# Performance work log

Measured on AMD Instinct MI355X. Metric: run time of the kernel, lower is better.

## Reference

```python
import jax, jax.numpy as jnp
import numpy as np

# q_config constants
W_IN, E_IN = 8, 4          # data_in_width, data_in_exponent_width
R_W = 6                     # data_r_width
W_OUT, E_OUT = 8, 4        # data_out_width, data_out_exponent_width (= data_n_width)
EXP_SUM_UF = 4              # exp_sum_underflow_bits
DIV_UF = 4                  # division_underflow_bits
W_DATA, E_DATA = 8, 4      # data_width, data_exponent_width

N, D = 8192, 2048


def integer_quantizer(x, width, frac_width):
    s = 2.0 ** frac_width
    lo, hi = -(2.0 ** (width - 1)), 2.0 ** (width - 1) - 1
    return jnp.clip(jnp.round(x * s), lo, hi) / s


def integer_floor_quantizer(x, width, frac_width):
    s = 2.0 ** frac_width
    lo, hi = -(2.0 ** (width - 1)), 2.0 ** (width - 1) - 1
    return jnp.clip(jnp.floor(x * s), lo, hi) / s


def mxint_quant(x, width, exponent_width):
    # MXInt block quantization with parallelism [1,1]: per-element shared exponent.
    e_hi, e_lo = 2.0 ** (exponent_width - 1) - 1, -(2.0 ** (exponent_width - 1))
    ax = jnp.abs(x)
    e = jnp.ceil(jnp.log2(jnp.where(ax == 0, 1.0, ax)))
    e = jnp.clip(e, e_lo, e_hi)
    scale = 2.0 ** (width - 1)
    m = jnp.clip(jnp.round(x * 2.0 ** (-e) * scale), -scale, scale - 1)
    qx = m * 2.0 ** e / scale
    return qx, m, e


def setup_inputs() -> dict:
    key = jax.random.key(0)
    x = jax.random.normal(key, (N, D), dtype=jnp.float32)
    return {"x": x}


def reference(x):
    # ---- MXIntHardwareExp: quantize input, range-reduce x = r + n*ln2 ----
    qx, _, _ = mxint_quant(x, W_IN, E_IN)
    log2e, _, _ = mxint_quant(jnp.float32(np.log2(np.e)), 8, 4)
    y = qx * log2e
    y = integer_floor_quantizer(y, E_OUT + R_W - 1, R_W - 1)
    n = jnp.floor(y)
    r = y - n                                # r in [0, 1)
    mexp = integer_quantizer(2.0 ** r, W_OUT, W_OUT - 2) * 2.0 ** (W_OUT - 2)
    eexp = n                                 # qexp = mexp * 2^eexp / 2^(W_OUT-2)

    # ---- exp_sum: exponent-aligned integer accumulation over dim 1 ----
    ms = (mexp * 2.0 ** EXP_SUM_UF).T        # [D, N]
    es = eexp.T                              # [D, N]

    def step(carry, me):
        out, emax = carry
        mi, ei = me
        new_emax = jnp.maximum(emax, ei)
        out = jnp.floor(out * 2.0 ** (emax - new_emax)) + jnp.floor(mi * 2.0 ** (ei - new_emax))
        return (out, new_emax), None

    (mexp_sum, eexp_sum), _ = jax.lax.scan(step, (ms[0], es[0]), (ms[1:], es[1:]))
    # mexp_sum, eexp_sum: [N]

    # ---- division: per-element mantissa integer division by the sum ----
    mout = jnp.floor(mexp * 2.0 ** (DIV_UF + EXP_SUM_UF) / mexp_sum[:, None])
    eout = eexp - eexp_sum[:, None]
    qout = mout * 2.0 ** eout / 2.0 ** DIV_UF
    qout, _, _ = mxint_quant(qout, W_DATA, E_DATA)
    return qout
```

## Files before the change

### kernel.cpp

```cpp
#include <hip/hip_runtime.h>


#define D_DIM 2048
#define TPB   128

__device__ __forceinline__ unsigned bmax4(unsigned x, unsigned y) {
    const unsigned d     = (x | 0x80808080u) - y;
    const unsigned flags = d & 0x80808080u;
    const unsigned mask  = (flags - (flags >> 7)) | flags;
    return (x & mask) | (y & ~mask);
}

__global__ __launch_bounds__(TPB, 6) void mxint_softmax_kernel(const float* __restrict__ x,
                                                               float* __restrict__ out) {
    const int t    = threadIdx.x;
    const int lane = t & 63;
    const int wid  = t >> 6;

    __shared__ unsigned short     s_pk[512];
    __shared__ float              s_fin[2][512];
    __shared__ int                s_rmax[2];
    __shared__ unsigned long long s_part[2];

    const size_t base = (size_t)blockIdx.x * D_DIM + wid * 1024 + lane * 4;
    float4 v[4];
#pragma unroll
    for (int i = 0; i < 4; ++i)
        v[i] = *(const float4*)(x + base + i * 256);

#pragma unroll
    for (int q = 0; q < 4; ++q) {
        const int idx = t + TPB * q;
        const float a = fmaf((float)(idx & 31), 0.03125f, 6.0f);
        const int  me = (int)rintf(__builtin_amdgcn_exp2f(a));
        s_pk[idx] = (unsigned short)(me << 4);
    }

    int yb[16];
    unsigned pe = 0;
#pragma unroll
    for (int i = 0; i < 4; ++i) {
        const float xs4[4] = {v[i].x, v[i].y, v[i].z, v[i].w};
        int rmax = 0;
#pragma unroll
        for (int k = 0; k < 4; ++k) {
            const unsigned b  = __float_as_uint(xs4[k]) & 0x7fffffffu;
            const unsigned tb = b + 0x7fffffu;
            const unsigned tc = min(max(tb, 0x3B800000u), 0x43000000u);
            const unsigned es = tc & 0xFF800000u;
            const float    su  = __uint_as_float(0x82800000u - es);
            const float    fac = __uint_as_float(es + 0xFF380000u);
            const float    mi  = __builtin_amdgcn_fmed3f(rintf(xs4[k] * su), -128.0f, 127.0f);
            int y = (int)fmaf(mi, fac, 256.0f);
            y = min(511, max(0, y));
            yb[4 * i + k] = y;
            rmax = max(rmax, y);
        }
        pe |= (unsigned)(rmax >> 5) << (8 * i);
    }

    unsigned s = pe;
#pragma unroll
    for (int d = 1; d < 64; d <<= 1) {
        const unsigned o = __shfl_up(s, d, 64);
        if (lane >= d) s = bmax4(s, o);
    }
    unsigned ex = __shfl_up(s, 1, 64);
    if (lane == 0) ex = 0;
    const unsigned bc = __shfl(s, 63, 64);
    const int wtot = max(max((int)(bc & 255u), (int)((bc >> 8) & 255u)),
                         max((int)((bc >> 16) & 255u), (int)(bc >> 24)));
    if (lane == 0) s_rmax[wid] = wtot;
    __syncthreads();

    const int c0 = wid ? s_rmax[0] : 0;

    unsigned partial = 0;
    int crun = c0;
#pragma unroll
    for (int i = 0; i < 4; ++i) {
        const int sx = (int)((ex >> (8 * i)) & 255u);
        int a = max(crun, sx);
#pragma unroll
        for (int k = 0; k < 4; ++k) {
            const int y = yb[4 * i + k];
            const int h = y >> 5;
            a = max(a, h);
            const unsigned me4 = s_pk[y];
            partial += (me4 >> (a - h)) << a;
        }
        crun = max(crun, (int)((bc >> (8 * i)) & 255u));
    }

    const unsigned ps = partial + __shfl_xor(partial, 1, 64);
    unsigned long long p64 = ps;
#pragma unroll
    for (int d = 2; d < 64; d <<= 1) p64 += __shfl_xor(p64, d, 64);
    if (lane == 0) s_part[wid] = p64;
    __syncthreads();

    const unsigned long long tot = s_part[0] + s_part[1];
    const int      Estar8 = max(s_rmax[0], s_rmax[1]);
    const unsigned msum   = (unsigned)(tot >> Estar8);
    const unsigned magic  = (unsigned)(274877906944.0 / (double)msum) + 1u;

    float* fin = s_fin[wid];
#pragma unroll
    for (int q = 0; q < 8; ++q) {
        const int      idx   = lane + 64 * q;
        const unsigned me4   = s_pk[idx];
        const unsigned mout  = __umulhi((unsigned)me4 << 4, magic) >> 6;
        const int      eoutn = Estar8 - (idx >> 5);
        const int      bl    = 32 - __clz((int)(mout | 1u));
        const int      pw2   = ((mout & (mout - 1u)) == 0u) ? 1 : 0;
        const int      clog  = bl - pw2;
        const int      sq    = min(7 - clog, 11 - eoutn);
        const int      rs    = 8 - sq;
        const unsigned u     = mout << 8;
        const unsigned bse   = u >> rs;
        const unsigned frac  = u & ((1u << rs) - 1u);
        const unsigned hlf   = 1u << (rs - 1);
        unsigned m2 = bse + (((frac > hlf) || (frac == hlf && (bse & 1u))) ? 1u : 0u);
        m2 = min(m2, 127u);
        const int ef = max(clog - eoutn - 4, -8);
        fin[idx] = (float)m2 * __uint_as_float((unsigned)(ef + 120) << 23);
    }

    float* orow = out + base;
#pragma unroll
    for (int i = 0; i < 4; ++i) {
        float r4[4];
#pragma unroll
        for (int k = 0; k < 4; ++k)
            r4[k] = fin[yb[4 * i + k]];
        const float4 o4 = {r4[0], r4[1], r4[2], r4[3]};
        *(float4*)(orow + i * 256) = o4;
    }
}

extern "C" void kernel_launch(void* const* d_in, const int* in_sizes, int n_in,
                              void* d_out, int out_size, void* d_ws, size_t ws_size,
                              hipStream_t stream) {
    const float* x = (const float*)d_in[0];
    float*       o = (float*)d_out;
    const int rows = in_sizes[0] / D_DIM;
    mxint_softmax_kernel<<<rows, TPB, 0, stream>>>(x, o);
}
```

Measured before the change: 110.8 us.

## Process four rows per block with register prefetch of next row

The grid shrinks to a fixed 2048 blocks, each looping over four rows strided by the block count. While the current row is computed, the next row's float4 loads are issued into registers, and the lookup table is built once per block instead of once per row. The goal is to hide global load latency and cut per-block setup cost. In exchange, register pressure rises, launch bounds drop from 6 to 4 blocks per CU, and the row count is hardcoded rather than taken from the input size.

```diff
diff --git a/kernel.cpp b/kernel.cpp
--- a/kernel.cpp
+++ b/kernel.cpp
@@ -3,6 +3,8 @@
 
 #define D_DIM 2048
 #define TPB   128
+#define NBLK  2048
+#define RPB   4
 
 __device__ __forceinline__ unsigned bmax4(unsigned x, unsigned y) {
     const unsigned d     = (x | 0x80808080u) - y;
@@ -11,7 +13,7 @@
     return (x & mask) | (y & ~mask);
 }
 
-__global__ __launch_bounds__(TPB, 6) void mxint_softmax_kernel(const float* __restrict__ x,
+__global__ __launch_bounds__(TPB, 4) void mxint_softmax_kernel(const float* __restrict__ x,
                                                                float* __restrict__ out) {
     const int t    = threadIdx.x;
     const int lane = t & 63;
@@ -19,14 +21,18 @@
 
     __shared__ unsigned short     s_pk[512];
     __shared__ float              s_fin[2][512];
-    __shared__ int                s_rmax[2];
-    __shared__ unsigned long long s_part[2];
+    __shared__ int                s_rmax[2][2];
+    __shared__ unsigned long long s_part[2][2];
 
-    const size_t base = (size_t)blockIdx.x * D_DIM + wid * 1024 + lane * 4;
+    const size_t off = (size_t)wid * 1024 + (size_t)lane * 4;
+
     float4 v[4];
+    {
+        const float* xr = x + (size_t)blockIdx.x * D_DIM + off;
 #pragma unroll
-    for (int i = 0; i < 4; ++i)
-        v[i] = *(const float4*)(x + base + i * 256);
+        for (int i = 0; i < 4; ++i)
+            v[i] = *(const float4*)(xr + i * 256);
+    }
 
 #pragma unroll
     for (int q = 0; q < 4; ++q) {
@@ -36,105 +42,124 @@
         s_pk[idx] = (unsigned short)(me << 4);
     }
 
-    int yb[16];
-    unsigned pe = 0;
+    for (int r = 0; r < RPB; ++r) {
+        const int row = blockIdx.x + r * NBLK;
+        const int pr  = r & 1;
+
+        float4 vn[4];
+        if (r + 1 < RPB) {
+            const float* xn = x + (size_t)(row + NBLK) * D_DIM + off;
 #pragma unroll
-    for (int i = 0; i < 4; ++i) {
-        const float xs4[4] = {v[i].x, v[i].y, v[i].z, v[i].w};
-        int rmax = 0;
+            for (int i = 0; i < 4; ++i)
+                vn[i] = *(const float4*)(xn + i * 256);
+        }
+
+        int yb[16];
+        unsigned pe = 0;
 #pragma unroll
-        for (int k = 0; k < 4; ++k) {
-            const unsigned b  = __float_as_uint(xs4[k]) & 0x7fffffffu;
-            const unsigned tb = b + 0x7fffffu;
-            const unsigned tc = min(max(tb, 0x3B800000u), 0x43000000u);
-            const unsigned es = tc & 0xFF800000u;
-            const float    su  = __uint_as_float(0x82800000u - es);
-            const float    fac = __uint_as_float(es + 0xFF380000u);
-            const float    mi  = __builtin_amdgcn_fmed3f(rintf(xs4[k] * su), -128.0f, 127.0f);
-            int y = (int)fmaf(mi, fac, 256.0f);
-            y = min(511, max(0, y));
-            yb[4 * i + k] = y;
-            rmax = max(rmax, y);
+        for (int i = 0; i < 4; ++i) {
+            const float xs4[4] = {v[i].x, v[i].y, v[i].z, v[i].w};
+            int rmax = 0;
+#pragma unroll
+            for (int k = 0; k < 4; ++k) {
+                const unsigned b  = __float_as_uint(xs4[k]) & 0x7fffffffu;
+                const unsigned tb = b + 0x7fffffu;
+                const unsigned tc = min(max(tb, 0x3B800000u), 0x43000000u);
+                const unsigned es = tc & 0xFF800000u;
+                const float    su  = __uint_as_float(0x82800000u - es);
+                const float    fac = __uint_as_float(es + 0xFF380000u);
+                const float    mi  = __builtin_amdgcn_fmed3f(rintf(xs4[k] * su),
+                                                             -128.0f, 127.0f);
+                int y = (int)fmaf(mi, fac, 256.0f);
+                y = min(511, max(0, y));
+                yb[4 * i + k] = y;
+                rmax = max(rmax, y);
+            }
+            pe |= (unsigned)(rmax >> 5) << (8 * i);
         }
-        pe |= (unsigned)(rmax >> 5) << (8 * i);
-    }
 
-    unsigned s = pe;
+        unsigned s = pe;
 #pragma unroll
-    for (int d = 1; d < 64; d <<= 1) {
-        const unsigned o = __shfl_up(s, d, 64);
-        if (lane >= d) s = bmax4(s, o);
-    }
-    unsigned ex = __shfl_up(s, 1, 64);
-    if (lane == 0) ex = 0;
-    const unsigned bc = __shfl(s, 63, 64);
-    const int wtot = max(max((int)(bc & 255u), (int)((bc >> 8) & 255u)),
-                         max((int)((bc >> 16) & 255u), (int)(bc >> 24)));
-    if (lane == 0) s_rmax[wid] = wtot;
-    __syncthreads();
+        for (int d = 1; d < 64; d <<= 1) {
+            const unsigned o = __shfl_up(s, d, 64);
+            if (lane >= d) s = bmax4(s, o);
+        }
+        unsigned ex = __shfl_up(s, 1, 64);
+        if (lane == 0) ex = 0;
+        const unsigned bc = __shfl(s, 63, 64);
+        const int wtot = max(max((int)(bc & 255u), (int)((bc >> 8) & 255u)),
+                             max((int)((bc >> 16) & 255u), (int)(bc >> 24)));
+        if (lane == 0) s_rmax[pr][wid] = wtot;
+        __syncthreads();
 
-    const int c0 = wid ? s_rmax[0] : 0;
+        const int c0 = wid ? s_rmax[pr][0] : 0;
 
-    unsigned partial = 0;
-    int crun = c0;
+        unsigned partial = 0;
+        int crun = c0;
 #pragma unroll
-    for (int i = 0; i < 4; ++i) {
-        const int sx = (int)((ex >> (8 * i)) & 255u);
-        int a = max(crun, sx);
+        for (int i = 0; i < 4; ++i) {
+            const int sx = (int)((ex >> (8 * i)) & 255u);
+            int a = max(crun, sx);
 #pragma unroll
-        for (int k = 0; k < 4; ++k) {
-            const int y = yb[4 * i + k];
-            const int h = y >> 5;
-            a = max(a, h);
-            const unsigned me4 = s_pk[y];
-            partial += (me4 >> (a - h)) << a;
+            for (int k = 0; k < 4; ++k) {
+                const int y = yb[4 * i + k];
+                const int h = y >> 5;
+                a = max(a, h);
+                const unsigned me4 = s_pk[y];
+                partial += (me4 >> (a - h)) << a;
+            }
+            crun = max(crun, (int)((bc >> (8 * i)) & 255u));
         }
-        crun = max(crun, (int)((bc >> (8 * i)) & 255u));
-    }
 
-    const unsigned ps = partial + __shfl_xor(partial, 1, 64);
-    unsigned long long p64 = ps;
+        const unsigned ps = partial + __shfl_xor(partial, 1, 64);
+        unsigned long long p64 = ps;
 #pragma unroll
-    for (int d = 2; d < 64; d <<= 1) p64 += __shfl_xor(p64, d, 64);
-    if (lane == 0) s_part[wid] = p64;
-    __syncthreads();
+        for (int d = 2; d < 64; d <<= 1) p64 += __shfl_xor(p64, d, 64);
+        if (lane == 0) s_part[pr][wid] = p64;
+        __syncthreads();
 
-    const unsigned long long tot = s_part[0] + s_part[1];
-    const int      Estar8 = max(s_rmax[0], s_rmax[1]);
-    const unsigned msum   = (unsigned)(tot >> Estar8);
-    const unsigned magic  = (unsigned)(274877906944.0 / (double)msum) + 1u;
+        const unsigned long long tot = s_part[pr][0] + s_part[pr][1];
+        const int      Estar8 = max(s_rmax[pr][0], s_rmax[pr][1]);
+        const unsigned msum   = (unsigned)(tot >> Estar8);
+        const unsigned magic  = (unsigned)(274877906944.0 / (double)msum) + 1u;
 
-    float* fin = s_fin[wid];
+        float* fin = s_fin[wid];
 #pragma unroll
-    for (int q = 0; q < 8; ++q) {
-        const int      idx   = lane + 64 * q;
-        const unsigned me4   = s_pk[idx];
-        const unsigned mout  = __umulhi((unsigned)me4 << 4, magic) >> 6;
-        const int      eoutn = Estar8 - (idx >> 5);
-        const int      bl    = 32 - __clz((int)(mout | 1u));
-        const int      pw2   = ((mout & (mout - 1u)) == 0u) ? 1 : 0;
-        const int      clog  = bl - pw2;
-        const int      sq    = min(7 - clog, 11 - eoutn);
-        const int      rs    = 8 - sq;
-        const unsigned u     = mout << 8;
-        const unsigned bse   = u >> rs;
-        const unsigned frac  = u & ((1u << rs) - 1u);
-        const unsigned hlf   = 1u << (rs - 1);
-        unsigned m2 = bse + (((frac > hlf) || (frac == hlf && (bse & 1u))) ? 1u : 0u);
-        m2 = min(m2, 127u);
-        const int ef = max(clog - eoutn - 4, -8);
-        fin[idx] = (float)m2 * __uint_as_float((unsigned)(ef + 120) << 23);
-    }
+        for (int q = 0; q < 8; ++q) {
+            const int      idx   = lane + 64 * q;
+            const unsigned me4   = s_pk[idx];
+            const unsigned mout  = __umulhi((unsigned)me4 << 4, magic) >> 6;
+            const int      eoutn = Estar8 - (idx >> 5);
+            const int      bl    = 32 - __clz((int)(mout | 1u));
+            const int      pw2   = ((mout & (mout - 1u)) == 0u) ? 1 : 0;
+            const int      clog  = bl - pw2;
+            const int      sq    = min(7 - clog, 11 - eoutn);
+            const int      rs    = 8 - sq;
+            const unsigned u     = mout << 8;
+            const unsigned bse   = u >> rs;
+            const unsigned frac  = u & ((1u << rs) - 1u);
+            const unsigned hlf   = 1u << (rs - 1);
+            unsigned m2 = bse + (((frac > hlf) || (frac == hlf && (bse & 1u))) ? 1u : 0u);
+            m2 = min(m2, 127u);
+            const int ef = max(clog - eoutn - 4, -8);
+            fin[idx] = (float)m2 * __uint_as_float((unsigned)(ef + 120) << 23);
+        }
 
-    float* orow = out + base;
+        float* orow = out + (size_t)row * D_DIM + off;
 #pragma unroll
-    for (int i = 0; i < 4; ++i) {
-        float r4[4];
+        for (int i = 0; i < 4; ++i) {
+            float r4[4];
 #pragma unroll
-        for (int k = 0; k < 4; ++k)
-            r4[k] = fin[yb[4 * i + k]];
-        const float4 o4 = {r4[0], r4[1], r4[2], r4[3]};
-        *(float4*)(orow + i * 256) = o4;
+            for (int k = 0; k < 4; ++k)
+                r4[k] = fin[yb[4 * i + k]];
+            const float4 o4 = {r4[0], r4[1], r4[2], r4[3]};
+            *(float4*)(orow + i * 256) = o4;
+        }
+
+        if (r + 1 < RPB) {
+#pragma unroll
+            for (int i = 0; i < 4; ++i) v[i] = vn[i];
+        }
     }
 }
 
@@ -143,6 +168,5 @@
                               hipStream_t stream) {
     const float* x = (const float*)d_in[0];
     float*       o = (float*)d_out;
-    const int rows = in_sizes[0] / D_DIM;
-    mxint_softmax_kernel<<<rows, TPB, 0, stream>>>(x, o);
+    mxint_softmax_kernel<<<NBLK, TPB, 0, stream>>>(x, o);
 }
```

After: 112.7 us. About the same (+1.7%).
